# Optimization experiments

Measured on AMD Instinct MI355X. Metric: run time of the kernel, lower is better.

The kernel has to match this reference:

```python
import jax, jax.numpy as jnp
import numpy as np

# dims
B, TQ, NQ, DQ = 2, 32, 196, 896      # batch, chunks, queries/chunk, slow-feat dim
T, H, W, CIN = 32, 8, 8, 4           # fast feature video dims
EMB = 1024                           # fast input mapping (kv) dim
HID = 512                            # cross_attn_hidden_dim
NH = 4                               # heads
HD = HID // NH                       # head dim = 128
HALF = HD // 2                       # 64 rotary freq channels
SEC = [22, 21, 21]                   # 3D rope sections (t,h,w) over the 64 freqs
FF = 2 * HID
OUT = 896
BASE = 10000.0
QGRID = 14                           # 196 = 14x14 query spatial grid
EPS = 1e-5


def _p(key, shape, scale=0.02):
    return (jax.random.normal(key, shape, dtype=jnp.float32) * scale)


def setup_inputs() -> dict:
    key = jax.random.key(0)
    ks = jax.random.split(key, 20)
    inp = {
        "x": jax.random.normal(ks[0], (B, T, H, W, CIN), dtype=jnp.float32),
        "slow_feats": jax.random.normal(ks[1], (B, TQ, NQ, DQ), dtype=jnp.float32),
        "frame_num": jnp.full((B,), T, dtype=jnp.int32),
        # query_input_mapping: 896 -> 512
        "Wq_in": _p(ks[2], (DQ, HID)), "bq_in": jnp.zeros((HID,), jnp.float32),
        # fast input_mapping (linear): 4 -> 1024
        "Wm": _p(ks[3], (CIN, EMB)), "bm": jnp.zeros((EMB,), jnp.float32),
        # cross-attn projections
        "Wq": _p(ks[4], (HID, HID)), "bq": jnp.zeros((HID,), jnp.float32),
        "Wk": _p(ks[5], (EMB, HID)), "bk": jnp.zeros((HID,), jnp.float32),
        "Wv": _p(ks[6], (EMB, HID)), "bv": jnp.zeros((HID,), jnp.float32),
        "Wo": _p(ks[7], (HID, HID)), "bo": jnp.zeros((HID,), jnp.float32),
        # decoder layer norms + FFN (dim_feedforward = 2*hidden)
        "g1": jnp.ones((HID,), jnp.float32), "be1": jnp.zeros((HID,), jnp.float32),
        "W1": _p(ks[8], (HID, FF)), "b1": jnp.zeros((FF,), jnp.float32),
        "W2": _p(ks[9], (FF, HID)), "b2": jnp.zeros((HID,), jnp.float32),
        "g2": jnp.ones((HID,), jnp.float32), "be2": jnp.zeros((HID,), jnp.float32),
        # output MLP (mlp_depth=2): 512 -> 1024 -> GELU -> 896
        "M1": _p(ks[10], (HID, 2 * HID)), "bm1": jnp.zeros((2 * HID,), jnp.float32),
        "M2": _p(ks[11], (2 * HID, OUT)), "bm2": jnp.zeros((OUT,), jnp.float32),
    }
    return inp


def _ln(x, g, b):
    m = x.mean(-1, keepdims=True)
    v = jnp.var(x, axis=-1, keepdims=True)
    return (x - m) * jax.lax.rsqrt(v + EPS) * g + b


def _rope_cos_sin(pos):
    # pos: (N,3) float (t,h,w). Qwen2-style inv_freq over head_dim=128.
    inv_freq = 1.0 / (BASE ** (jnp.arange(0, HD, 2, dtype=jnp.float32) / HD))  # (64,)
    sel = jnp.asarray([0] * SEC[0] + [1] * SEC[1] + [2] * SEC[2])              # (64,)
    freqs = pos[:, sel] * inv_freq                                             # (N,64)
    emb = jnp.concatenate([freqs, freqs], axis=-1)                             # (N,128)
    return jnp.cos(emb), jnp.sin(emb)


def _rot_half(x):
    return jnp.concatenate([-x[..., HALF:], x[..., :HALF]], axis=-1)


def _positions():
    # query tokens: (chunk t, 14x14 grid)
    qt = jnp.repeat(jnp.arange(TQ), NQ)
    qg = jnp.tile(jnp.arange(NQ), TQ)
    q_pos = jnp.stack([qt, qg // QGRID, qg % QGRID], axis=-1).astype(jnp.float32)  # (6272,3)
    # kv tokens: (frame t, HxW grid)
    kt = jnp.repeat(jnp.arange(T), H * W)
    kg = jnp.tile(jnp.arange(H * W), T)
    k_pos = jnp.stack([kt, kg // W, kg % W], axis=-1).astype(jnp.float32)          # (2048,3)
    return q_pos, k_pos


def _forward(x, slow_feats, Wq_in, bq_in, Wm, bm, Wq, bq, Wk, bk, Wv, bv,
             Wo, bo, g1, be1, W1, b1, W2, b2, g2, be2, M1, bm1, M2, bm2):
    q_pos, k_pos = _positions()
    cos_q, sin_q = _rope_cos_sin(q_pos)   # (Nq,128)
    cos_k, sin_k = _rope_cos_sin(k_pos)   # (Nk,128)
    scale = 1.0 / jnp.sqrt(jnp.float32(HD))

    def per_sample(xi, si):
        # slow feats -> queries: (32,196,896) -> (6272,512)
        q_in = (si.reshape(TQ * NQ, DQ) @ Wq_in + bq_in)
        # fast feats -> kv tokens: (T,H,W,Cin) -> (2048,1024)
        kv = (xi.reshape(T * H * W, CIN) @ Wm + bm)
        # projections -> heads
        q = (q_in @ Wq + bq).reshape(-1, NH, HD)
        k = (kv @ Wk + bk).reshape(-1, NH, HD)
        v = (kv @ Wv + bv).reshape(-1, NH, HD)
        # 3D RoPE on q and k
        q = q * cos_q[:, None, :] + _rot_half(q) * sin_q[:, None, :]
        k = k * cos_k[:, None, :] + _rot_half(k) * sin_k[:, None, :]
        # cross attention
        attn = jnp.einsum('qhd,khd->hqk', q, k) * scale
        attn = jax.nn.softmax(attn, axis=-1)
        o = jnp.einsum('hqk,khd->qhd', attn, v).reshape(-1, HID)
        o = o @ Wo + bo
        # residual + norm + FFN + norm (post-norm decoder layer)
        h = _ln(q_in + o, g1, be1)
        ff = jax.nn.gelu(h @ W1 + b1) @ W2 + b2
        h = _ln(h + ff, g2, be2)
        # output MLP: Linear -> GELU -> Linear
        y = jax.nn.gelu(h @ M1 + bm1) @ M2 + bm2
        return y  # (6272, 896)

    return jax.vmap(per_sample)(x, slow_feats)  # (B, 6272, 896)


def reference(x, slow_feats, frame_num, Wq_in, bq_in, Wm, bm, Wq, bq, Wk, bk,
              Wv, bv, Wo, bo, g1, be1, W1, b1, W2, b2, g2, be2, M1, bm1, M2, bm2):
    # frame_num is the valid-frame count per sample; here all samples are full
    # length (frame_num == T), so no KV masking is needed.
    del frame_num
    return _forward(x, slow_feats, Wq_in, bq_in, Wm, bm, Wq, bq, Wk, bk, Wv, bv,
                    Wo, bo, g1, be1, W1, b1, W2, b2, g2, be2, M1, bm1, M2, bm2)
```

## Files before the change

### kernel.cpp

```cpp
#include <hip/hip_runtime.h>
#include <cstdint>
#include <cstddef>

#define BATCH 2
#define MQ 12544
#define ROWS_Q 6272
#define MK 4096
#define ROWS_K 2048
#define HID 512
#define NH 4
#define HD 128
#define EMB 1024
#define DQ 896
#define FF 1024
#define OUTD 896

typedef __bf16 bf16;
typedef unsigned int u32;
typedef bf16 bf16x8 __attribute__((ext_vector_type(8)));
typedef bf16 bf16x4 __attribute__((ext_vector_type(4)));
typedef float f32x4 __attribute__((ext_vector_type(4)));

enum { OP_BIAS = 0, OP_GELU = 1, OP_RES = 2 };

__device__ __forceinline__ float gelu_tanh(float x) {
    float x3 = x * x * x;
    return 0.5f * x * (1.0f + tanhf(0.7978845608028654f * (x + 0.044715f * x3)));
}

__device__ __forceinline__ void gld16(const bf16* g, bf16* l) {
    __builtin_amdgcn_global_load_lds(
        (const __attribute__((address_space(1))) unsigned int*)g,
        (__attribute__((address_space(3))) unsigned int*)l, 16, 0, 0);
}

__device__ __forceinline__ u32 pack_bf16(float a, float b) {
    union { bf16 h[2]; u32 w; } u;
    u.h[0] = (bf16)a; u.h[1] = (bf16)b;
    return u.w;
}

template <int OP, bool WF32, bool WB16>
__global__ __launch_bounds__(256) void mgemm(
    const bf16* __restrict__ A, const bf16* __restrict__ Bt,
    const float* __restrict__ bias, const float* __restrict__ res,
    float* __restrict__ Cf, bf16* __restrict__ Cb, int M, int N, int K)
{
    __shared__ __align__(16) bf16 As[128 * 32];
    __shared__ __align__(16) bf16 Bs[128 * 32];
    const int tid  = threadIdx.x;
    const int m0   = blockIdx.y * 128;
    const int n0   = blockIdx.x * 128;
    const int wave = tid >> 6, lane = tid & 63;
    const int wm = (wave >> 1) * 64, wn = (wave & 1) * 64;

    f32x4 acc[4][4] = {};

    const int srow = tid >> 2;
    const int scol = (tid & 3) * 8;
    const bf16* Ag = A  + (size_t)(m0 + srow) * K + scol;
    const bf16* Bg = Bt + (size_t)(n0 + srow) * K + scol;
    bf16* Al = &As[tid * 8];
    bf16* Bl = &Bs[tid * 8];
    const size_t half = (size_t)64 * K;

    const int fr = lane & 15;
    const int kq = (lane >> 4) * 8;
    const bf16* pa = &As[(wm + fr) * 32 + kq];
    const bf16* pb = &Bs[(wn + fr) * 32 + kq];

    for (int k0 = 0; k0 < K; k0 += 32) {
        gld16(Ag + k0,        Al);
        gld16(Ag + k0 + half, Al + 64 * 32);
        gld16(Bg + k0,        Bl);
        gld16(Bg + k0 + half, Bl + 64 * 32);
        __syncthreads();

        bf16x8 af[4], bfr[4];
        #pragma unroll
        for (int i = 0; i < 4; ++i) af[i]  = *(const bf16x8*)(pa + i * 16 * 32);
        #pragma unroll
        for (int j = 0; j < 4; ++j) bfr[j] = *(const bf16x8*)(pb + j * 16 * 32);
        #pragma unroll
        for (int i = 0; i < 4; ++i)
            #pragma unroll
            for (int j = 0; j < 4; ++j)
                acc[i][j] = __builtin_amdgcn_mfma_f32_16x16x32_bf16(
                    af[i], bfr[j], acc[i][j], 0, 0, 0);
        __syncthreads();
    }

    const int colb = n0 + wn + (lane & 15);
    const int rowb = m0 + wm + (lane >> 4) * 4;
    #pragma unroll
    for (int i = 0; i < 4; ++i) {
        #pragma unroll
        for (int j = 0; j < 4; ++j) {
            const int c = colb + j * 16;
            const float bj = bias[c];
            #pragma unroll
            for (int r = 0; r < 4; ++r) {
                const int m = rowb + i * 16 + r;
                float v = acc[i][j][r] + bj;
                if (OP == OP_GELU) v = gelu_tanh(v);
                if (OP == OP_RES)  v += res[(size_t)m * N + c];
                if (WF32) Cf[(size_t)m * N + c] = v;
                if (WB16) Cb[(size_t)m * N + c] = (bf16)v;
            }
        }
    }
}

template <int OP, bool WF32, bool WB16>
__global__ __launch_bounds__(256) void mgemm64(
    const bf16* __restrict__ A, const bf16* __restrict__ Bt,
    const float* __restrict__ bias, const float* __restrict__ res,
    float* __restrict__ Cf, bf16* __restrict__ Cb, int M, int N, int K)
{
    __shared__ __align__(16) bf16 As[64 * 32];
    __shared__ __align__(16) bf16 Bs[128 * 32];
    const int tid  = threadIdx.x;
    const int m0   = blockIdx.y * 64;
    const int n0   = blockIdx.x * 128;
    const int wave = tid >> 6, lane = tid & 63;
    const int wm = (wave >> 1) * 32, wn = (wave & 1) * 64;

    f32x4 acc[2][4] = {};

    const int srow = tid >> 2;
    const int scol = (tid & 3) * 8;
    const bf16* Ag = A  + (size_t)(m0 + srow) * K + scol;
    const bf16* Bg = Bt + (size_t)(n0 + srow) * K + scol;
    bf16* Al = &As[tid * 8];
    bf16* Bl = &Bs[tid * 8];
    const size_t half = (size_t)64 * K;

    const int fr = lane & 15;
    const int kq = (lane >> 4) * 8;
    const bf16* pa = &As[(wm + fr) * 32 + kq];
    const bf16* pb = &Bs[(wn + fr) * 32 + kq];

    for (int k0 = 0; k0 < K; k0 += 32) {
        gld16(Ag + k0,        Al);
        gld16(Bg + k0,        Bl);
        gld16(Bg + k0 + half, Bl + 64 * 32);
        __syncthreads();

        bf16x8 af[2], bfr[4];
        #pragma unroll
        for (int i = 0; i < 2; ++i) af[i]  = *(const bf16x8*)(pa + i * 16 * 32);
        #pragma unroll
        for (int j = 0; j < 4; ++j) bfr[j] = *(const bf16x8*)(pb + j * 16 * 32);
        #pragma unroll
        for (int i = 0; i < 2; ++i)
            #pragma unroll
            for (int j = 0; j < 4; ++j)
                acc[i][j] = __builtin_amdgcn_mfma_f32_16x16x32_bf16(
                    af[i], bfr[j], acc[i][j], 0, 0, 0);
        __syncthreads();
    }

    const int colb = n0 + wn + (lane & 15);
    const int rowb = m0 + wm + (lane >> 4) * 4;
    #pragma unroll
    for (int i = 0; i < 2; ++i) {
        #pragma unroll
        for (int j = 0; j < 4; ++j) {
            const int c = colb + j * 16;
            const float bj = bias[c];
            #pragma unroll
            for (int r = 0; r < 4; ++r) {
                const int m = rowb + i * 16 + r;
                float v = acc[i][j][r] + bj;
                if (OP == OP_GELU) v = gelu_tanh(v);
                if (OP == OP_RES)  v += res[(size_t)m * N + c];
                if (WF32) Cf[(size_t)m * N + c] = v;
                if (WB16) Cb[(size_t)m * N + c] = (bf16)v;
            }
        }
    }
}

struct TDesc { const float* src; bf16* dst; int K; int N; int tile0; };
struct TDescs { TDesc d[9]; };

__global__ __launch_bounds__(256) void transpose_all(TDescs td)
{
    __shared__ float t[32][33];
    const int blk = blockIdx.x;
    int i = 0;
    #pragma unroll
    for (int j = 1; j < 9; ++j) if (blk >= td.d[j].tile0) i = j;
    const float* src = td.d[i].src;
    bf16* dst = td.d[i].dst;
    const int K = td.d[i].K, N = td.d[i].N;
    const int local = blk - td.d[i].tile0;
    const int ntx = N >> 5;
    const int bx = local % ntx, by = local / ntx;
    const int x = threadIdx.x & 31, y = threadIdx.x >> 5;
    #pragma unroll
    for (int p = 0; p < 32; p += 8)
        t[y + p][x] = src[(size_t)(by * 32 + y + p) * N + bx * 32 + x];
    __syncthreads();
    #pragma unroll
    for (int p = 0; p < 32; p += 8)
        dst[(size_t)(bx * 32 + y + p) * K + by * 32 + x] = (bf16)t[x][y + p];
}

__global__ __launch_bounds__(256) void cvt_kernel(
    const float* __restrict__ in, bf16* __restrict__ out, int n4)
{
    int i = blockIdx.x * 256 + threadIdx.x;
    if (i >= n4) return;
    float4 v = ((const float4*)in)[i];
    out[4 * i + 0] = (bf16)v.x;
    out[4 * i + 1] = (bf16)v.y;
    out[4 * i + 2] = (bf16)v.z;
    out[4 * i + 3] = (bf16)v.w;
}

__global__ __launch_bounds__(256) void kv_kernel(
    const float* __restrict__ x, const float* __restrict__ Wm,
    const float* __restrict__ bm, bf16* __restrict__ kv)
{
    int idx = blockIdx.x * 256 + threadIdx.x;
    int r = idx >> 10, n = idx & 1023;
    float4 xv = *(const float4*)(x + (size_t)r * 4);
    float v = bm[n] + xv.x * Wm[n] + xv.y * Wm[1024 + n]
                    + xv.z * Wm[2048 + n] + xv.w * Wm[3072 + n];
    kv[idx] = (bf16)v;
}

__global__ __launch_bounds__(256) void rope_b_kernel(
    const bf16* __restrict__ in, bf16* __restrict__ out,
    int tok, int gdiv, int wdiv, int total, float sc, int istr, int icoff)
{
    int idx = blockIdx.x * 256 + threadIdx.x;
    if (idx >= total) return;
    int row = idx >> 7;
    int r2 = idx & 127;
    int h = r2 >> 5;
    int j2 = r2 & 31;
    int j = 2 * j2;
    int n = row % tok;
    int t = n / gdiv;
    int g = n % gdiv;
    int gh = g / wdiv;
    int gw = g % wdiv;
    float pa = (j < 22) ? (float)t : (j < 43) ? (float)gh : (float)gw;
    int j1 = j + 1;
    float pb = (j1 < 22) ? (float)t : (j1 < 43) ? (float)gh : (float)gw;
    float fra = pa * exp2f(-(float)j  * 0.20762050593045954f);
    float frb = pb * exp2f(-(float)j1 * 0.20762050593045954f);
    float ca = cosf(fra), sa = sinf(fra);
    float cb = cosf(frb), sb = sinf(frb);
    size_t ibase = (size_t)row * istr + icoff + (size_t)h * 128 + j;
    size_t obase = (size_t)row * 512 + (size_t)h * 128 + j;
    union { u32 w; bf16 e[2]; } ua, ub;
    ua.w = *(const u32*)(in + ibase);
    ub.w = *(const u32*)(in + ibase + 64);
    float x1a = (float)ua.e[0], x1b = (float)ua.e[1];
    float x2a = (float)ub.e[0], x2b = (float)ub.e[1];
    *(u32*)(out + obase)      = pack_bf16((x1a * ca - x2a * sa) * sc,
                                          (x1b * cb - x2b * sb) * sc);
    *(u32*)(out + obase + 64) = pack_bf16((x2a * ca + x1a * sa) * sc,
                                          (x2b * cb + x1b * sb) * sc);
}

__global__ __launch_bounds__(256) void vt_tiled(
    const bf16* __restrict__ kv16, bf16* __restrict__ vt)
{
    __shared__ bf16 t[64][72];
    const int tt = blockIdx.x * 64;
    const int d0 = blockIdx.y * 64;
    const int bh = blockIdx.z;
    const int b = bh >> 2, h = bh & 3;
    const int rr = threadIdx.x >> 4;
    const int cc = (threadIdx.x & 15) * 4;
    #pragma unroll
    for (int p = 0; p < 4; ++p) {
        int r = rr + p * 16;
        *(bf16x4*)&t[r][cc] = *(const bf16x4*)
            (kv16 + (size_t)(b * ROWS_K + tt + r) * 1024 + 512 + h * 128 + d0 + cc);
    }
    __syncthreads();
    #pragma unroll
    for (int p = 0; p < 4; ++p) {
        int r = rr + p * 16;
        bf16x4 v;
        v[0] = t[cc + 0][r]; v[1] = t[cc + 1][r];
        v[2] = t[cc + 2][r]; v[3] = t[cc + 3][r];
        *(bf16x4*)(vt + (size_t)bh * HD * ROWS_K + (size_t)(d0 + r) * ROWS_K + tt + cc) = v;
    }
}

__global__ __launch_bounds__(256) void ln_kernel(
    float* __restrict__ xb, const float* __restrict__ g,
    const float* __restrict__ be, bf16* __restrict__ out16)
{
    int wave = threadIdx.x >> 6, lane = threadIdx.x & 63;
    size_t row = (size_t)blockIdx.x * 4 + wave;
    float* xp = xb + row * 512;
    float4 a = ((const float4*)xp)[lane];
    float4 b = ((const float4*)xp)[lane + 64];
    float s  = a.x + a.y + a.z + a.w + b.x + b.y + b.z + b.w;
    float sq = a.x*a.x + a.y*a.y + a.z*a.z + a.w*a.w
             + b.x*b.x + b.y*b.y + b.z*b.z + b.w*b.w;
    #pragma unroll
    for (int off = 32; off; off >>= 1) {
        s  += __shfl_xor(s, off);
        sq += __shfl_xor(sq, off);
    }
    float mean = s * (1.0f / 512.0f);
    float var  = sq * (1.0f / 512.0f) - mean * mean;
    float rstd = rsqrtf(var + 1e-5f);
    float4 gv1 = ((const float4*)g)[lane],  gv2 = ((const float4*)g)[lane + 64];
    float4 bv1 = ((const float4*)be)[lane], bv2 = ((const float4*)be)[lane + 64];
    a.x = (a.x - mean) * rstd * gv1.x + bv1.x;
    a.y = (a.y - mean) * rstd * gv1.y + bv1.y;
    a.z = (a.z - mean) * rstd * gv1.z + bv1.z;
    a.w = (a.w - mean) * rstd * gv1.w + bv1.w;
    b.x = (b.x - mean) * rstd * gv2.x + bv2.x;
    b.y = (b.y - mean) * rstd * gv2.y + bv2.y;
    b.z = (b.z - mean) * rstd * gv2.z + bv2.z;
    b.w = (b.w - mean) * rstd * gv2.w + bv2.w;
    ((float4*)xp)[lane]      = a;
    ((float4*)xp)[lane + 64] = b;
    bf16* op = out16 + row * 512;
    *(u32*)(op + lane * 4)       = pack_bf16(a.x, a.y);
    *(u32*)(op + lane * 4 + 2)   = pack_bf16(a.z, a.w);
    *(u32*)(op + 256 + lane * 4)     = pack_bf16(b.x, b.y);
    *(u32*)(op + 256 + lane * 4 + 2) = pack_bf16(b.z, b.w);
}

__global__ __launch_bounds__(256, 2) void mattn_kernel(
    const bf16* __restrict__ qs, const bf16* __restrict__ ks,
    const bf16* __restrict__ vt, bf16* __restrict__ outb)
{
    __shared__ __align__(16) char smem[35840];
    bf16* Ksh = (bf16*)smem;
    bf16* Vsh = (bf16*)(smem + 17408);

    const int tid = threadIdx.x;
    const int wave = tid >> 6, lane = tid & 63;
    const int quad = lane >> 4, c = lane & 15;
    const int bid = blockIdx.x;
    const int qt = bid % 49;
    const int h  = (bid / 49) & 3;
    const int b  = bid / 196;

    const int q0 = qt * 128 + wave * 32;
    const bf16* qg = qs + (size_t)(b * ROWS_Q + q0) * HID + h * HD;
    const bf16* kg = ks + (size_t)(b * ROWS_K) * HID + h * HD;
    const bf16* vg = vt + (size_t)(b * NH + h) * HD * ROWS_K;

    bf16x8 qf[2][4];
    #pragma unroll
    for (int n = 0; n < 2; ++n)
        #pragma unroll
        for (int s = 0; s < 4; ++s)
            qf[n][s] = *(const bf16x8*)(qg + (size_t)(n * 16 + c) * HID + s * 32 + quad * 8);

    f32x4 o[8][2] = {};
    float m_i[2] = {-1e30f, -1e30f}, l_i[2] = {0.0f, 0.0f};

    const int st_t = tid >> 2;
    const int st_d = (tid & 3) * 32;
    const int sv_d = tid >> 1;
    const int sv_t = (tid & 1) * 32;

    for (int kt = 0; kt < 32; ++kt) {
        __syncthreads();
        {
            const bf16* src = kg + (size_t)(kt * 64 + st_t) * HID + st_d;
            bf16* dst = Ksh + st_t * 136 + st_d;
            #pragma unroll
            for (int i = 0; i < 4; ++i)
                *(bf16x8*)(dst + i * 8) = *(const bf16x8*)(src + i * 8);
        }
        {
            const bf16* src = vg + (size_t)sv_d * ROWS_K + kt * 64 + sv_t;
            bf16* dst = Vsh + sv_d * 72 + sv_t;
            #pragma unroll
            for (int i = 0; i < 4; ++i)
                *(bf16x8*)(dst + i * 8) = *(const bf16x8*)(src + i * 8);
        }
        __syncthreads();

        f32x4 s[4][2] = {};
        #pragma unroll
        for (int ksi = 0; ksi < 4; ++ksi) {
            bf16x8 kf[4];
            #pragma unroll
            for (int mi = 0; mi < 4; ++mi)
                kf[mi] = *(const bf16x8*)(Ksh + (mi * 16 + c) * 136 + ksi * 32 + quad * 8);
            #pragma unroll
            for (int mi = 0; mi < 4; ++mi)
                #pragma unroll
                for (int n = 0; n < 2; ++n)
                    s[mi][n] = __builtin_amdgcn_mfma_f32_16x16x32_bf16(
                        kf[mi], qf[n][ksi], s[mi][n], 0, 0, 0);
        }

        float alpha[2];
        #pragma unroll
        for (int n = 0; n < 2; ++n) {
            float mx = -1e30f;
            #pragma unroll
            for (int mi = 0; mi < 4; ++mi)
                #pragma unroll
                for (int r = 0; r < 4; ++r) mx = fmaxf(mx, s[mi][n][r]);
            mx = fmaxf(mx, __shfl_xor(mx, 16));
            mx = fmaxf(mx, __shfl_xor(mx, 32));
            float mn = fmaxf(m_i[n], mx);
            alpha[n] = __expf(m_i[n] - mn);
            m_i[n] = mn;
            float sm = 0.0f;
            #pragma unroll
            for (int mi = 0; mi < 4; ++mi)
                #pragma unroll
                for (int r = 0; r < 4; ++r) {
                    float p = __expf(s[mi][n][r] - mn);
                    s[mi][n][r] = p;
                    sm += p;
                }
            sm += __shfl_xor(sm, 16);
            sm += __shfl_xor(sm, 32);
            l_i[n] = l_i[n] * alpha[n] + sm;
            #pragma unroll
            for (int md = 0; md < 8; ++md) {
                o[md][n][0] *= alpha[n]; o[md][n][1] *= alpha[n];
                o[md][n][2] *= alpha[n]; o[md][n][3] *= alpha[n];
            }
        }

        u32 pk[4][2][2];
        #pragma unroll
        for (int mi = 0; mi < 4; ++mi)
            #pragma unroll
            for (int n = 0; n < 2; ++n) {
                pk[mi][n][0] = pack_bf16(s[mi][n][0], s[mi][n][1]);
                pk[mi][n][1] = pack_bf16(s[mi][n][2], s[mi][n][3]);
            }
        bf16x8 pf[2][2];
        #pragma unroll
        for (int kst = 0; kst < 2; ++kst)
            #pragma unroll
            for (int n = 0; n < 2; ++n) {
                union { bf16x8 v8; u32 d[4]; } u;
                #pragma unroll
                for (int dw = 0; dw < 4; ++dw) {
                    int srcl = ((quad & 1) * 2 + (dw >> 1)) * 16 + c;
                    u32 lo = (u32)__shfl((int)pk[2 * kst][n][dw & 1], srcl);
                    u32 hi = (u32)__shfl((int)pk[2 * kst + 1][n][dw & 1], srcl);
                    u.d[dw] = (quad >= 2) ? hi : lo;
                }
                pf[kst][n] = u.v8;
            }

        #pragma unroll
        for (int kst = 0; kst < 2; ++kst)
            #pragma unroll
            for (int md = 0; md < 8; ++md) {
                bf16x8 vf = *(const bf16x8*)(Vsh + (md * 16 + c) * 72 + kst * 32 + quad * 8);
                #pragma unroll
                for (int n = 0; n < 2; ++n)
                    o[md][n] = __builtin_amdgcn_mfma_f32_16x16x32_bf16(
                        vf, pf[kst][n], o[md][n], 0, 0, 0);
            }
    }

    __syncthreads();
    bf16* Osh = (bf16*)smem + wave * (32 * 136);
    float inv[2] = {1.0f / l_i[0], 1.0f / l_i[1]};
    #pragma unroll
    for (int md = 0; md < 8; ++md)
        #pragma unroll
        for (int n = 0; n < 2; ++n)
            #pragma unroll
            for (int hh = 0; hh < 2; ++hh) {
                u32 w = pack_bf16(o[md][n][2 * hh] * inv[n], o[md][n][2 * hh + 1] * inv[n]);
                int d = md * 16 + quad * 4 + 2 * hh;
                int qq = n * 16 + c;
                *(u32*)(Osh + qq * 136 + d) = w;
            }
    __syncthreads();
    bf16* og = outb + (size_t)(b * ROWS_Q + q0) * HID + h * HD;
    #pragma unroll
    for (int i = 0; i < 8; ++i) {
        int idx = i * 64 + lane;
        int qq = idx >> 4;
        int ch = idx & 15;
        bf16x8 vv = *(const bf16x8*)(Osh + qq * 136 + ch * 8);
        *(bf16x8*)(og + (size_t)qq * HID + ch * 8) = vv;
    }
}

extern "C" void kernel_launch(void* const* d_in, const int* in_sizes, int n_in,
                              void* d_out, int out_size, void* d_ws, size_t ws_size,
                              hipStream_t stream)
{
    const float* x     = (const float*)d_in[0];
    const float* slow  = (const float*)d_in[1];
    const float* Wq_in = (const float*)d_in[3];
    const float* bq_in = (const float*)d_in[4];
    const float* Wm    = (const float*)d_in[5];
    const float* bm    = (const float*)d_in[6];
    const float* Wq    = (const float*)d_in[7];
    const float* bq    = (const float*)d_in[8];
    const float* Wk    = (const float*)d_in[9];
    const float* bk    = (const float*)d_in[10];
    const float* Wv    = (const float*)d_in[11];
    const float* bv    = (const float*)d_in[12];
    const float* Wo    = (const float*)d_in[13];
    const float* bo    = (const float*)d_in[14];
    const float* g1    = (const float*)d_in[15];
    const float* be1   = (const float*)d_in[16];
    const float* W1    = (const float*)d_in[17];
    const float* b1    = (const float*)d_in[18];
    const float* W2    = (const float*)d_in[19];
    const float* b2    = (const float*)d_in[20];
    const float* g2    = (const float*)d_in[21];
    const float* be2   = (const float*)d_in[22];
    const float* M1    = (const float*)d_in[23];
    const float* bm1   = (const float*)d_in[24];
    const float* M2    = (const float*)d_in[25];
    const float* bm2   = (const float*)d_in[26];
    float* out = (float*)d_out;

    float* q_in_f = (float*)d_ws;
    float* ob     = q_in_f + (size_t)MQ * HID;
    float* bkv    = ob + (size_t)MQ * HID;
    bf16* shared_b = (bf16*)(bkv + 1024);
    bf16* q_in_b = shared_b + (size_t)MQ * FF;
    bf16* kv_b   = q_in_b + (size_t)MQ * HID;
    bf16* h_b    = kv_b + (size_t)MK * EMB;
    bf16* q16    = h_b + (size_t)MQ * HID;
    bf16* kv16   = q16 + (size_t)MQ * HID;
    bf16* qbt    = kv16 + (size_t)MK * EMB;
    bf16* kbt    = qbt + (size_t)MQ * HID;
    bf16* Vt     = kbt + (size_t)MK * HID;
    bf16* Wq_in_t = Vt + (size_t)8 * HD * ROWS_K;
    bf16* Wq_t  = Wq_in_t + 512 * 896;
    bf16* kvw_t = Wq_t + 512 * 512;
    bf16* Wo_t  = kvw_t + 1024 * 1024;
    bf16* W1_t  = Wo_t + 512 * 512;
    bf16* W2_t  = W1_t + 1024 * 512;
    bf16* M1_t  = W2_t + 512 * 1024;
    bf16* M2_t  = M1_t + 1024 * 512;
    bf16* slow_b = shared_b;
    bf16* attn_b = shared_b;
    bf16* ff1_b  = shared_b;
    bf16* m1_b   = shared_b;

    dim3 blk(256);

    TDescs td;
    int t0 = 0;
    auto set = [&](int i, const float* s, bf16* d, int K, int N) {
        td.d[i] = {s, d, K, N, t0};
        t0 += (N / 32) * (K / 32);
    };
    set(0, Wq_in, Wq_in_t, 896, 512);
    set(1, Wq,    Wq_t,    512, 512);
    set(2, Wk,    kvw_t,              1024, 512);
    set(3, Wv,    kvw_t + 512 * 1024, 1024, 512);
    set(4, Wo,    Wo_t,    512, 512);
    set(5, W1,    W1_t,    512, 1024);
    set(6, W2,    W2_t,    1024, 512);
    set(7, M1,    M1_t,    512, 1024);
    set(8, M2,    M2_t,    1024, 896);
    transpose_all<<<t0, blk, 0, stream>>>(td);

    hipMemcpyAsync(bkv,       bk, 512 * sizeof(float), hipMemcpyDeviceToDevice, stream);
    hipMemcpyAsync(bkv + 512, bv, 512 * sizeof(float), hipMemcpyDeviceToDevice, stream);

    cvt_kernel<<<(MQ * DQ / 4 + 255) / 256, blk, 0, stream>>>(slow, slow_b, MQ * DQ / 4);
    kv_kernel<<<(MK * EMB) / 256, blk, 0, stream>>>(x, Wm, bm, kv_b);

    mgemm64<OP_BIAS, true, true><<<dim3(4, 196), blk, 0, stream>>>(
        slow_b, Wq_in_t, bq_in, nullptr, q_in_f, q_in_b, MQ, HID, DQ);
    mgemm64<OP_BIAS, false, true><<<dim3(4, 196), blk, 0, stream>>>(
        q_in_b, Wq_t, bq, nullptr, nullptr, q16, MQ, HID, HID);
    mgemm64<OP_BIAS, false, true><<<dim3(8, 64), blk, 0, stream>>>(
        kv_b, kvw_t, bkv, nullptr, nullptr, kv16, MK, 1024, EMB);
    rope_b_kernel<<<(MQ * 128 + 255) / 256, blk, 0, stream>>>(
        q16, qbt, ROWS_Q, 196, 14, MQ * 128, 0.08838834764831843f, 512, 0);
    rope_b_kernel<<<(MK * 128 + 255) / 256, blk, 0, stream>>>(
        kv16, kbt, ROWS_K, 64, 8, MK * 128, 1.0f, 1024, 0);
    vt_tiled<<<dim3(32, 2, 8), blk, 0, stream>>>(kv16, Vt);
    mattn_kernel<<<dim3(392), blk, 0, stream>>>(qbt, kbt, Vt, attn_b);
    mgemm64<OP_RES, true, false><<<dim3(4, 196), blk, 0, stream>>>(
        attn_b, Wo_t, bo, q_in_f, ob, nullptr, MQ, HID, HID);
    ln_kernel<<<MQ / 4, blk, 0, stream>>>(ob, g1, be1, h_b);
    mgemm<OP_GELU, false, true><<<dim3(8, 98), blk, 0, stream>>>(
        h_b, W1_t, b1, nullptr, nullptr, ff1_b, MQ, FF, HID);
    mgemm64<OP_RES, true, false><<<dim3(4, 196), blk, 0, stream>>>(
        ff1_b, W2_t, b2, ob, q_in_f, nullptr, MQ, HID, FF);
    ln_kernel<<<MQ / 4, blk, 0, stream>>>(q_in_f, g2, be2, h_b);
    mgemm<OP_GELU, false, true><<<dim3(8, 98), blk, 0, stream>>>(
        h_b, M1_t, bm1, nullptr, nullptr, m1_b, MQ, 2 * HID, HID);
    mgemm<OP_BIAS, true, false><<<dim3(7, 98), blk, 0, stream>>>(
        m1_b, M2_t, bm2, nullptr, out, nullptr, MQ, OUTD, 2 * HID);
}
```

Baseline: 582.3 us.

## Split attention blocks into 8 waves of 16 queries with padded LDS strides

The attention kernel now runs 512 threads per block, with each wave handling 16 query rows instead of 32. This halves per-wave register state (one output accumulator set and softmax state) and doubles the number of waves sharing each K/V tile, to raise occupancy and latency hiding. LDS row strides are padded (140/76) to reduce bank conflicts. The online softmax also skips the rescale when no row maximum grows, using a wave-wide vote. The trade-off is more waves doing the same QK and V fragment LDS reads per tile, so total LDS read traffic per query grows.

```diff
diff --git a/kernel.cpp b/kernel.cpp
--- a/kernel.cpp
+++ b/kernel.cpp
@@ -333,13 +333,17 @@
     *(u32*)(op + 256 + lane * 4 + 2) = pack_bf16(b.z, b.w);
 }
 
-__global__ __launch_bounds__(256, 2) void mattn_kernel(
+#define KS 140
+#define VS 76
+#define OS 140
+
+__global__ __launch_bounds__(512, 4) void mattn_kernel(
     const bf16* __restrict__ qs, const bf16* __restrict__ ks,
     const bf16* __restrict__ vt, bf16* __restrict__ outb)
 {
-    __shared__ __align__(16) char smem[35840];
+    __shared__ __align__(16) char smem[37376];
     bf16* Ksh = (bf16*)smem;
-    bf16* Vsh = (bf16*)(smem + 17408);
+    bf16* Vsh = (bf16*)(smem + 17920);
 
     const int tid = threadIdx.x;
     const int wave = tid >> 6, lane = tid & 63;
@@ -349,149 +353,135 @@
     const int h  = (bid / 49) & 3;
     const int b  = bid / 196;
 
-    const int q0 = qt * 128 + wave * 32;
+    const int q0 = qt * 128 + wave * 16;
     const bf16* qg = qs + (size_t)(b * ROWS_Q + q0) * HID + h * HD;
     const bf16* kg = ks + (size_t)(b * ROWS_K) * HID + h * HD;
     const bf16* vg = vt + (size_t)(b * NH + h) * HD * ROWS_K;
 
-    bf16x8 qf[2][4];
-    #pragma unroll
-    for (int n = 0; n < 2; ++n)
-        #pragma unroll
-        for (int s = 0; s < 4; ++s)
-            qf[n][s] = *(const bf16x8*)(qg + (size_t)(n * 16 + c) * HID + s * 32 + quad * 8);
-
-    f32x4 o[8][2] = {};
-    float m_i[2] = {-1e30f, -1e30f}, l_i[2] = {0.0f, 0.0f};
-
-    const int st_t = tid >> 2;
-    const int st_d = (tid & 3) * 32;
-    const int sv_d = tid >> 1;
-    const int sv_t = (tid & 1) * 32;
+    bf16x8 qf[4];
+    #pragma unroll
+    for (int s = 0; s < 4; ++s)
+        qf[s] = *(const bf16x8*)(qg + (size_t)c * HID + s * 32 + quad * 8);
+
+    f32x4 o[8] = {};
+    float m_i = -1e30f, l_i = 0.0f;
+
+    const int st_t = tid >> 3;
+    const int st_d = (tid & 7) * 16;
+    const int sv_d = tid >> 2;
+    const int sv_t = (tid & 3) * 16;
 
     for (int kt = 0; kt < 32; ++kt) {
         __syncthreads();
         {
             const bf16* src = kg + (size_t)(kt * 64 + st_t) * HID + st_d;
-            bf16* dst = Ksh + st_t * 136 + st_d;
-            #pragma unroll
-            for (int i = 0; i < 4; ++i)
+            bf16* dst = Ksh + st_t * KS + st_d;
+            #pragma unroll
+            for (int i = 0; i < 2; ++i)
                 *(bf16x8*)(dst + i * 8) = *(const bf16x8*)(src + i * 8);
         }
         {
             const bf16* src = vg + (size_t)sv_d * ROWS_K + kt * 64 + sv_t;
-            bf16* dst = Vsh + sv_d * 72 + sv_t;
-            #pragma unroll
-            for (int i = 0; i < 4; ++i)
+            bf16* dst = Vsh + sv_d * VS + sv_t;
+            #pragma unroll
+            for (int i = 0; i < 2; ++i)
                 *(bf16x8*)(dst + i * 8) = *(const bf16x8*)(src + i * 8);
         }
         __syncthreads();
 
-        f32x4 s[4][2] = {};
+        f32x4 s[4] = {};
         #pragma unroll
         for (int ksi = 0; ksi < 4; ++ksi) {
             bf16x8 kf[4];
             #pragma unroll
             for (int mi = 0; mi < 4; ++mi)
-                kf[mi] = *(const bf16x8*)(Ksh + (mi * 16 + c) * 136 + ksi * 32 + quad * 8);
+                kf[mi] = *(const bf16x8*)(Ksh + (mi * 16 + c) * KS + ksi * 32 + quad * 8);
             #pragma unroll
             for (int mi = 0; mi < 4; ++mi)
-                #pragma unroll
-                for (int n = 0; n < 2; ++n)
-                    s[mi][n] = __builtin_amdgcn_mfma_f32_16x16x32_bf16(
-                        kf[mi], qf[n][ksi], s[mi][n], 0, 0, 0);
-        }
-
-        float alpha[2];
-        #pragma unroll
-        for (int n = 0; n < 2; ++n) {
-            float mx = -1e30f;
-            #pragma unroll
-            for (int mi = 0; mi < 4; ++mi)
-                #pragma unroll
-                for (int r = 0; r < 4; ++r) mx = fmaxf(mx, s[mi][n][r]);
-            mx = fmaxf(mx, __shfl_xor(mx, 16));
-            mx = fmaxf(mx, __shfl_xor(mx, 32));
-            float mn = fmaxf(m_i[n], mx);
-            alpha[n] = __expf(m_i[n] - mn);
-            m_i[n] = mn;
-            float sm = 0.0f;
-            #pragma unroll
-            for (int mi = 0; mi < 4; ++mi)
-                #pragma unroll
-                for (int r = 0; r < 4; ++r) {
-                    float p = __expf(s[mi][n][r] - mn);
-                    s[mi][n][r] = p;
-                    sm += p;
-                }
-            sm += __shfl_xor(sm, 16);
-            sm += __shfl_xor(sm, 32);
-            l_i[n] = l_i[n] * alpha[n] + sm;
+                s[mi] = __builtin_amdgcn_mfma_f32_16x16x32_bf16(
+                    kf[mi], qf[ksi], s[mi], 0, 0, 0);
+        }
+
+        float mx = -1e30f;
+        #pragma unroll
+        for (int mi = 0; mi < 4; ++mi)
+            #pragma unroll
+            for (int r = 0; r < 4; ++r) mx = fmaxf(mx, s[mi][r]);
+        mx = fmaxf(mx, __shfl_xor(mx, 16));
+        mx = fmaxf(mx, __shfl_xor(mx, 32));
+        if (!__all(mx <= m_i)) {
+            float mn = fmaxf(m_i, mx);
+            float alpha = __expf(m_i - mn);
+            m_i = mn;
+            l_i *= alpha;
             #pragma unroll
             for (int md = 0; md < 8; ++md) {
-                o[md][n][0] *= alpha[n]; o[md][n][1] *= alpha[n];
-                o[md][n][2] *= alpha[n]; o[md][n][3] *= alpha[n];
+                o[md][0] *= alpha; o[md][1] *= alpha;
+                o[md][2] *= alpha; o[md][3] *= alpha;
             }
         }
-
-        u32 pk[4][2][2];
+        float sm = 0.0f;
         #pragma unroll
         for (int mi = 0; mi < 4; ++mi)
             #pragma unroll
-            for (int n = 0; n < 2; ++n) {
-                pk[mi][n][0] = pack_bf16(s[mi][n][0], s[mi][n][1]);
-                pk[mi][n][1] = pack_bf16(s[mi][n][2], s[mi][n][3]);
+            for (int r = 0; r < 4; ++r) {
+                float p = __expf(s[mi][r] - m_i);
+                s[mi][r] = p;
+                sm += p;
             }
-        bf16x8 pf[2][2];
+        sm += __shfl_xor(sm, 16);
+        sm += __shfl_xor(sm, 32);
+        l_i += sm;
+
+        u32 pk[4][2];
+        #pragma unroll
+        for (int mi = 0; mi < 4; ++mi) {
+            pk[mi][0] = pack_bf16(s[mi][0], s[mi][1]);
+            pk[mi][1] = pack_bf16(s[mi][2], s[mi][3]);
+        }
+        bf16x8 pf[2];
+        #pragma unroll
+        for (int kst = 0; kst < 2; ++kst) {
+            union { bf16x8 v8; u32 d[4]; } u;
+            #pragma unroll
+            for (int dw = 0; dw < 4; ++dw) {
+                int srcl = ((quad & 1) * 2 + (dw >> 1)) * 16 + c;
+                u32 lo = (u32)__shfl((int)pk[2 * kst][dw & 1], srcl);
+                u32 hi = (u32)__shfl((int)pk[2 * kst + 1][dw & 1], srcl);
+                u.d[dw] = (quad >= 2) ? hi : lo;
+            }
+            pf[kst] = u.v8;
+        }
+
         #pragma unroll
         for (int kst = 0; kst < 2; ++kst)
             #pragma unroll
-            for (int n = 0; n < 2; ++n) {
-                union { bf16x8 v8; u32 d[4]; } u;
-                #pragma unroll
-                for (int dw = 0; dw < 4; ++dw) {
-                    int srcl = ((quad & 1) * 2 + (dw >> 1)) * 16 + c;
-                    u32 lo = (u32)__shfl((int)pk[2 * kst][n][dw & 1], srcl);
-                    u32 hi = (u32)__shfl((int)pk[2 * kst + 1][n][dw & 1], srcl);
-                    u.d[dw] = (quad >= 2) ? hi : lo;
-                }
-                pf[kst][n] = u.v8;
+            for (int md = 0; md < 8; ++md) {
+                bf16x8 vf = *(const bf16x8*)(Vsh + (md * 16 + c) * VS + kst * 32 + quad * 8);
+                o[md] = __builtin_amdgcn_mfma_f32_16x16x32_bf16(
+                    vf, pf[kst], o[md], 0, 0, 0);
             }
-
-        #pragma unroll
-        for (int kst = 0; kst < 2; ++kst)
-            #pragma unroll
-            for (int md = 0; md < 8; ++md) {
-                bf16x8 vf = *(const bf16x8*)(Vsh + (md * 16 + c) * 72 + kst * 32 + quad * 8);
-                #pragma unroll
-                for (int n = 0; n < 2; ++n)
-                    o[md][n] = __builtin_amdgcn_mfma_f32_16x16x32_bf16(
-                        vf, pf[kst][n], o[md][n], 0, 0, 0);
-            }
     }
 
     __syncthreads();
-    bf16* Osh = (bf16*)smem + wave * (32 * 136);
-    float inv[2] = {1.0f / l_i[0], 1.0f / l_i[1]};
+    bf16* Osh = (bf16*)smem + wave * (16 * OS);
+    float inv = 1.0f / l_i;
     #pragma unroll
     for (int md = 0; md < 8; ++md)
         #pragma unroll
-        for (int n = 0; n < 2; ++n)
-            #pragma unroll
-            for (int hh = 0; hh < 2; ++hh) {
-                u32 w = pack_bf16(o[md][n][2 * hh] * inv[n], o[md][n][2 * hh + 1] * inv[n]);
-                int d = md * 16 + quad * 4 + 2 * hh;
-                int qq = n * 16 + c;
-                *(u32*)(Osh + qq * 136 + d) = w;
-            }
+        for (int hh = 0; hh < 2; ++hh) {
+            u32 w = pack_bf16(o[md][2 * hh] * inv, o[md][2 * hh + 1] * inv);
+            int d = md * 16 + quad * 4 + 2 * hh;
+            *(u32*)(Osh + c * OS + d) = w;
+        }
     __syncthreads();
-    bf16* og = outb + (size_t)(b * ROWS_Q + q0) * HID + h * HD;
-    #pragma unroll
-    for (int i = 0; i < 8; ++i) {
-        int idx = i * 64 + lane;
+    bf16* og = outb + (size_t)(b * ROWS_Q + qt * 128) * HID + h * HD;
+    #pragma unroll
+    for (int i = 0; i < 4; ++i) {
+        int idx = i * 512 + tid;
         int qq = idx >> 4;
         int ch = idx & 15;
-        bf16x8 vv = *(const bf16x8*)(Osh + qq * 136 + ch * 8);
+        bf16x8 vv = *(const bf16x8*)((bf16*)smem + (qq >> 4) * (16 * OS) + (qq & 15) * OS + ch * 8);
         *(bf16x8*)(og + (size_t)qq * HID + ch * 8) = vv;
     }
 }
@@ -589,7 +579,7 @@
     rope_b_kernel<<<(MK * 128 + 255) / 256, blk, 0, stream>>>(
         kv16, kbt, ROWS_K, 64, 8, MK * 128, 1.0f, 1024, 0);
     vt_tiled<<<dim3(32, 2, 8), blk, 0, stream>>>(kv16, Vt);
-    mattn_kernel<<<dim3(392), blk, 0, stream>>>(qbt, kbt, Vt, attn_b);
+    mattn_kernel<<<dim3(392), dim3(512), 0, stream>>>(qbt, kbt, Vt, attn_b);
     mgemm64<OP_RES, true, false><<<dim3(4, 196), blk, 0, stream>>>(
         attn_b, Wo_t, bo, q_in_f, ob, nullptr, MQ, HID, HID);
     ln_kernel<<<MQ / 4, blk, 0, stream>>>(ob, g1, be1, h_b);
```

After: 989.5 us. 1.7x slower.

## Double-buffer K/V tiles via register prefetch and skip redundant softmax rescale

Applied to the files above, without the earlier changes.

The attention kernel now holds two LDS buffers. It prefetches the next K/V tile from global memory into registers while the current tile is being computed, then writes it into the alternate buffer, so global load latency is hidden behind the MFMA work. The online-softmax rescale of the output accumulators is skipped when no row maximum grew anywhere in the wave. The LDS row strides also change (136→140, 72→76) to alter bank mapping. In exchange, LDS use per block roughly doubles, to about 73KB, which may limit the two-blocks-per-CU occupancy target, and register pressure rises from the prefetch buffers.

```diff
diff --git a/kernel.cpp b/kernel.cpp
--- a/kernel.cpp
+++ b/kernel.cpp
@@ -333,13 +333,18 @@
     *(u32*)(op + 256 + lane * 4 + 2) = pack_bf16(b.z, b.w);
 }
 
+#define KS 140
+#define VS 76
+#define OS 140
+#define KBYTES 17920
+#define VBYTES 19456
+#define BUFB 37376
+
 __global__ __launch_bounds__(256, 2) void mattn_kernel(
     const bf16* __restrict__ qs, const bf16* __restrict__ ks,
     const bf16* __restrict__ vt, bf16* __restrict__ outb)
 {
-    __shared__ __align__(16) char smem[35840];
-    bf16* Ksh = (bf16*)smem;
-    bf16* Vsh = (bf16*)(smem + 17408);
+    __shared__ __align__(16) char smem[2 * BUFB];
 
     const int tid = threadIdx.x;
     const int wave = tid >> 6, lane = tid & 63;
@@ -368,24 +373,37 @@
     const int st_d = (tid & 3) * 32;
     const int sv_d = tid >> 1;
     const int sv_t = (tid & 1) * 32;
+    const bf16* ksrc = kg + (size_t)st_t * HID + st_d;
+    const bf16* vsrc = vg + (size_t)sv_d * ROWS_K + sv_t;
+
+    bf16x8 rK[4], rV[4];
+    #pragma unroll
+    for (int i = 0; i < 4; ++i) rK[i] = *(const bf16x8*)(ksrc + i * 8);
+    #pragma unroll
+    for (int i = 0; i < 4; ++i) rV[i] = *(const bf16x8*)(vsrc + i * 8);
+    {
+        bf16* Kd = (bf16*)smem + st_t * KS + st_d;
+        bf16* Vd = (bf16*)(smem + KBYTES) + sv_d * VS + sv_t;
+        #pragma unroll
+        for (int i = 0; i < 4; ++i) *(bf16x8*)(Kd + i * 8) = rK[i];
+        #pragma unroll
+        for (int i = 0; i < 4; ++i) *(bf16x8*)(Vd + i * 8) = rV[i];
+    }
+    __syncthreads();
 
     for (int kt = 0; kt < 32; ++kt) {
-        __syncthreads();
-        {
-            const bf16* src = kg + (size_t)(kt * 64 + st_t) * HID + st_d;
-            bf16* dst = Ksh + st_t * 136 + st_d;
-            #pragma unroll
-            for (int i = 0; i < 4; ++i)
-                *(bf16x8*)(dst + i * 8) = *(const bf16x8*)(src + i * 8);
-        }
-        {
-            const bf16* src = vg + (size_t)sv_d * ROWS_K + kt * 64 + sv_t;
-            bf16* dst = Vsh + sv_d * 72 + sv_t;
-            #pragma unroll
-            for (int i = 0; i < 4; ++i)
-                *(bf16x8*)(dst + i * 8) = *(const bf16x8*)(src + i * 8);
-        }
-        __syncthreads();
+        const int cur = kt & 1;
+        const bf16* Ksh = (const bf16*)(smem + cur * BUFB);
+        const bf16* Vsh = (const bf16*)(smem + cur * BUFB + KBYTES);
+
+        if (kt < 31) {
+            const bf16* s1 = ksrc + (size_t)(kt + 1) * 64 * HID;
+            const bf16* s2 = vsrc + (kt + 1) * 64;
+            #pragma unroll
+            for (int i = 0; i < 4; ++i) rK[i] = *(const bf16x8*)(s1 + i * 8);
+            #pragma unroll
+            for (int i = 0; i < 4; ++i) rV[i] = *(const bf16x8*)(s2 + i * 8);
+        }
 
         f32x4 s[4][2] = {};
         #pragma unroll
@@ -393,7 +411,7 @@
             bf16x8 kf[4];
             #pragma unroll
             for (int mi = 0; mi < 4; ++mi)
-                kf[mi] = *(const bf16x8*)(Ksh + (mi * 16 + c) * 136 + ksi * 32 + quad * 8);
+                kf[mi] = *(const bf16x8*)(Ksh + (mi * 16 + c) * KS + ksi * 32 + quad * 8);
             #pragma unroll
             for (int mi = 0; mi < 4; ++mi)
                 #pragma unroll
@@ -402,36 +420,46 @@
                         kf[mi], qf[n][ksi], s[mi][n], 0, 0, 0);
         }
 
-        float alpha[2];
+        float mx[2];
         #pragma unroll
         for (int n = 0; n < 2; ++n) {
-            float mx = -1e30f;
+            float m = -1e30f;
             #pragma unroll
             for (int mi = 0; mi < 4; ++mi)
                 #pragma unroll
-                for (int r = 0; r < 4; ++r) mx = fmaxf(mx, s[mi][n][r]);
-            mx = fmaxf(mx, __shfl_xor(mx, 16));
-            mx = fmaxf(mx, __shfl_xor(mx, 32));
-            float mn = fmaxf(m_i[n], mx);
-            alpha[n] = __expf(m_i[n] - mn);
-            m_i[n] = mn;
+                for (int r = 0; r < 4; ++r) m = fmaxf(m, s[mi][n][r]);
+            m = fmaxf(m, __shfl_xor(m, 16));
+            m = fmaxf(m, __shfl_xor(m, 32));
+            mx[n] = m;
+        }
+        if (!__all((mx[0] <= m_i[0]) && (mx[1] <= m_i[1]))) {
+            #pragma unroll
+            for (int n = 0; n < 2; ++n) {
+                float mn = fmaxf(m_i[n], mx[n]);
+                float alpha = __expf(m_i[n] - mn);
+                m_i[n] = mn;
+                l_i[n] *= alpha;
+                #pragma unroll
+                for (int md = 0; md < 8; ++md) {
+                    o[md][n][0] *= alpha; o[md][n][1] *= alpha;
+                    o[md][n][2] *= alpha; o[md][n][3] *= alpha;
+                }
+            }
+        }
+        #pragma unroll
+        for (int n = 0; n < 2; ++n) {
             float sm = 0.0f;
             #pragma unroll
             for (int mi = 0; mi < 4; ++mi)
                 #pragma unroll
                 for (int r = 0; r < 4; ++r) {
-                    float p = __expf(s[mi][n][r] - mn);
+                    float p = __expf(s[mi][n][r] - m_i[n]);
                     s[mi][n][r] = p;
                     sm += p;
                 }
             sm += __shfl_xor(sm, 16);
             sm += __shfl_xor(sm, 32);
-            l_i[n] = l_i[n] * alpha[n] + sm;
-            #pragma unroll
-            for (int md = 0; md < 8; ++md) {
-                o[md][n][0] *= alpha[n]; o[md][n][1] *= alpha[n];
-                o[md][n][2] *= alpha[n]; o[md][n][3] *= alpha[n];
-            }
+            l_i[n] += sm;
         }
 
         u32 pk[4][2][2];
@@ -462,16 +490,27 @@
         for (int kst = 0; kst < 2; ++kst)
             #pragma unroll
             for (int md = 0; md < 8; ++md) {
-                bf16x8 vf = *(const bf16x8*)(Vsh + (md * 16 + c) * 72 + kst * 32 + quad * 8);
+                bf16x8 vf = *(const bf16x8*)(Vsh + (md * 16 + c) * VS + kst * 32 + quad * 8);
                 #pragma unroll
                 for (int n = 0; n < 2; ++n)
                     o[md][n] = __builtin_amdgcn_mfma_f32_16x16x32_bf16(
                         vf, pf[kst][n], o[md][n], 0, 0, 0);
             }
+
+        if (kt < 31) {
+            __syncthreads();
+            bf16* Kd = (bf16*)(smem + (cur ^ 1) * BUFB) + st_t * KS + st_d;
+            bf16* Vd = (bf16*)(smem + (cur ^ 1) * BUFB + KBYTES) + sv_d * VS + sv_t;
+            #pragma unroll
+            for (int i = 0; i < 4; ++i) *(bf16x8*)(Kd + i * 8) = rK[i];
+            #pragma unroll
+            for (int i = 0; i < 4; ++i) *(bf16x8*)(Vd + i * 8) = rV[i];
+            __syncthreads();
+        }
     }
 
     __syncthreads();
-    bf16* Osh = (bf16*)smem + wave * (32 * 136);
+    bf16* Osh = (bf16*)smem + wave * (32 * OS);
     float inv[2] = {1.0f / l_i[0], 1.0f / l_i[1]};
     #pragma unroll
     for (int md = 0; md < 8; ++md)
@@ -482,7 +521,7 @@
                 u32 w = pack_bf16(o[md][n][2 * hh] * inv[n], o[md][n][2 * hh + 1] * inv[n]);
                 int d = md * 16 + quad * 4 + 2 * hh;
                 int qq = n * 16 + c;
-                *(u32*)(Osh + qq * 136 + d) = w;
+                *(u32*)(Osh + qq * OS + d) = w;
             }
     __syncthreads();
     bf16* og = outb + (size_t)(b * ROWS_Q + q0) * HID + h * HD;
@@ -491,7 +530,7 @@
         int idx = i * 64 + lane;
         int qq = idx >> 4;
         int ch = idx & 15;
-        bf16x8 vv = *(const bf16x8*)(Osh + qq * 136 + ch * 8);
+        bf16x8 vv = *(const bf16x8*)(Osh + qq * OS + ch * 8);
         *(bf16x8*)(og + (size_t)qq * HID + ch * 8) = vv;
     }
 }
```

Result: slower. 800.9 us (+37.5%).

## Split attention KV range into two partitions and merge with a combine kernel

Applied to the files above, without the earlier changes.

The attention kernel now splits the 2048-key range into two halves, so the grid doubles from 392 to 784 blocks. Each half writes normalized partial outputs plus per-row max and sum to reused workspace buffers. A new combine kernel merges the two partials with log-sum-exp weights. This targets low occupancy from only 392 blocks on a GPU with many CUs, at the cost of an extra kernel launch, extra global traffic for the partials, and a second bf16 rounding.

```diff
diff --git a/kernel.cpp b/kernel.cpp
--- a/kernel.cpp
+++ b/kernel.cpp
@@ -335,7 +335,9 @@
 
 __global__ __launch_bounds__(256, 2) void mattn_kernel(
     const bf16* __restrict__ qs, const bf16* __restrict__ ks,
-    const bf16* __restrict__ vt, bf16* __restrict__ outb)
+    const bf16* __restrict__ vt, bf16* __restrict__ op0,
+    bf16* __restrict__ op1, float* __restrict__ mbuf,
+    float* __restrict__ lbuf)
 {
     __shared__ __align__(16) char smem[35840];
     bf16* Ksh = (bf16*)smem;
@@ -347,7 +349,9 @@
     const int bid = blockIdx.x;
     const int qt = bid % 49;
     const int h  = (bid / 49) & 3;
-    const int b  = bid / 196;
+    const int rest = bid / 196;
+    const int b    = rest & 1;
+    const int part = rest >> 1;
 
     const int q0 = qt * 128 + wave * 32;
     const bf16* qg = qs + (size_t)(b * ROWS_Q + q0) * HID + h * HD;
@@ -369,7 +373,8 @@
     const int sv_d = tid >> 1;
     const int sv_t = (tid & 1) * 32;
 
-    for (int kt = 0; kt < 32; ++kt) {
+    const int kt0 = part * 16;
+    for (int kt = kt0; kt < kt0 + 16; ++kt) {
         __syncthreads();
         {
             const bf16* src = kg + (size_t)(kt * 64 + st_t) * HID + st_d;
@@ -470,6 +475,15 @@
             }
     }
 
+    if (quad == 0) {
+        #pragma unroll
+        for (int n = 0; n < 2; ++n) {
+            int row = b * ROWS_Q + q0 + n * 16 + c;
+            mbuf[(part * 4 + h) * MQ + row] = m_i[n];
+            lbuf[(part * 4 + h) * MQ + row] = l_i[n];
+        }
+    }
+
     __syncthreads();
     bf16* Osh = (bf16*)smem + wave * (32 * 136);
     float inv[2] = {1.0f / l_i[0], 1.0f / l_i[1]};
@@ -485,7 +499,8 @@
                 *(u32*)(Osh + qq * 136 + d) = w;
             }
     __syncthreads();
-    bf16* og = outb + (size_t)(b * ROWS_Q + q0) * HID + h * HD;
+    bf16* opb = part ? op1 : op0;
+    bf16* og = opb + (size_t)(b * ROWS_Q + q0) * HID + h * HD;
     #pragma unroll
     for (int i = 0; i < 8; ++i) {
         int idx = i * 64 + lane;
@@ -494,6 +509,32 @@
         bf16x8 vv = *(const bf16x8*)(Osh + qq * 136 + ch * 8);
         *(bf16x8*)(og + (size_t)qq * HID + ch * 8) = vv;
     }
+}
+
+__global__ __launch_bounds__(256) void comb_kernel(
+    const bf16* __restrict__ o0, const bf16* __restrict__ o1,
+    const float* __restrict__ mbuf, const float* __restrict__ lbuf,
+    bf16* __restrict__ outb)
+{
+    int idx = blockIdx.x * 256 + threadIdx.x;
+    int row = idx >> 6;
+    int col8 = idx & 63;
+    int h = col8 >> 4;
+    int mli = h * MQ + row;
+    float m1 = mbuf[mli],          l1 = lbuf[mli];
+    float m2 = mbuf[4 * MQ + mli], l2 = lbuf[4 * MQ + mli];
+    float mm = fmaxf(m1, m2);
+    float a1 = l1 * __expf(m1 - mm), a2 = l2 * __expf(m2 - mm);
+    float inv = 1.0f / (a1 + a2);
+    float w1 = a1 * inv, w2 = a2 * inv;
+    size_t off = (size_t)idx * 8;
+    bf16x8 v1 = *(const bf16x8*)(o0 + off);
+    bf16x8 v2 = *(const bf16x8*)(o1 + off);
+    bf16x8 r;
+    #pragma unroll
+    for (int j = 0; j < 8; ++j)
+        r[j] = (bf16)((float)v1[j] * w1 + (float)v2[j] * w2);
+    *(bf16x8*)(outb + off) = r;
 }
 
 extern "C" void kernel_launch(void* const* d_in, const int* in_sizes, int n_in,
@@ -553,6 +594,11 @@
     bf16* ff1_b  = shared_b;
     bf16* m1_b   = shared_b;
 
+    bf16* opart0 = q16;
+    bf16* opart1 = q_in_b;
+    float* mlm   = (float*)kv16;
+    float* mll   = mlm + 8 * MQ;
+
     dim3 blk(256);
 
     TDescs td;
@@ -589,7 +635,8 @@
     rope_b_kernel<<<(MK * 128 + 255) / 256, blk, 0, stream>>>(
         kv16, kbt, ROWS_K, 64, 8, MK * 128, 1.0f, 1024, 0);
     vt_tiled<<<dim3(32, 2, 8), blk, 0, stream>>>(kv16, Vt);
-    mattn_kernel<<<dim3(392), blk, 0, stream>>>(qbt, kbt, Vt, attn_b);
+    mattn_kernel<<<dim3(784), blk, 0, stream>>>(qbt, kbt, Vt, opart0, opart1, mlm, mll);
+    comb_kernel<<<dim3(MQ * 64 / 256), blk, 0, stream>>>(opart0, opart1, mlm, mll, attn_b);
     mgemm64<OP_RES, true, false><<<dim3(4, 196), blk, 0, stream>>>(
         attn_b, Wo_t, bo, q_in_f, ob, nullptr, MQ, HID, HID);
     ln_kernel<<<MQ / 4, blk, 0, stream>>>(ob, g1, be1, h_b);
```

Result: no change. 585.8 us (+0.6%).
